# Kernel optimization log

Hardware: AMD Instinct MI355X
Metric: run time of the kernel (lower is better)

Reference implementation:

```python
import jax, jax.numpy as jnp
import numpy as np

# ---- dims (match init_kwargs / input_specs) ----
N = 20000      # nodes
E = 640000     # edges (avg degree 32)
A = 64         # num_node_feats (0e attrs)
F = 32         # num_features per irrep
B = 8          # num_bessel
H = 64         # radial MLP hidden
L = 2          # num_layers
NPATH = 5      # TP paths: s*Y0->0e, s*Y1->1e, v*Y0->1e, v.Y1->0e, v x Y1->1e
RMAX = 5.0
P = 6          # num_polynomial_cutoff
AVG = 32.0     # avg_num_neighbours


def setup_inputs() -> dict:
    key = jax.random.key(0)
    ks = jax.random.split(key, 11)
    node_attrs = jax.random.normal(ks[0], (N, A), jnp.float32)
    coordinates = jax.random.normal(ks[1], (N, 3), jnp.float32)
    edge_index = jax.random.randint(ks[2], (2, E), 0, N, dtype=jnp.int32)
    # learned params (e3nn-style fan-in init)
    node_emb_W = jax.random.normal(ks[3], (A, F), jnp.float32) * A ** -0.5
    rad_W1 = jax.random.normal(ks[4], (L, B, H), jnp.float32) * B ** -0.5
    rad_b1 = jnp.zeros((L, H), jnp.float32)
    rad_W2 = jax.random.normal(ks[5], (L, H, NPATH * F), jnp.float32) * H ** -0.5
    lin_Ws = jax.random.normal(ks[6], (L, F, 2 * F), jnp.float32) * F ** -0.5
    lin_Wv = jax.random.normal(ks[7], (L, F, F), jnp.float32) * F ** -0.5
    sc_Ws = jax.random.normal(ks[8], (L, F, A, 2 * F), jnp.float32) * (F * A) ** -0.5
    sc_Wv = jax.random.normal(ks[9], (L, F, A, F), jnp.float32) * (F * A) ** -0.5
    return {"node_attrs": node_attrs, "coordinates": coordinates, "edge_index": edge_index,
            "node_emb_W": node_emb_W, "rad_W1": rad_W1, "rad_b1": rad_b1, "rad_W2": rad_W2,
            "lin_Ws": lin_Ws, "lin_Wv": lin_Wv, "sc_Ws": sc_Ws, "sc_Wv": sc_Wv}


def _nequip_forward(node_attrs, coordinates, node_emb_W, rad_W1, rad_b1, rad_W2,
                    lin_Ws, lin_Wv, sc_Ws, sc_Wv, edge_index):
    snd, rcv = edge_index[0], edge_index[1]
    vec = coordinates[snd] - coordinates[rcv]                    # [E,3]
    r = jnp.sqrt(jnp.sum(vec * vec, -1) + 1e-12)                 # [E]
    unit = vec / r[:, None]
    x = r / RMAX
    # Bessel radial basis * polynomial cutoff (p=6)
    n = jnp.arange(1, B + 1, dtype=jnp.float32)
    bessel = jnp.sqrt(2.0 / RMAX) * jnp.sin(n[None, :] * jnp.pi * x[:, None]) / r[:, None]
    c1 = -(P + 1) * (P + 2) / 2.0
    c2 = float(P * (P + 2))
    c3 = -P * (P + 1) / 2.0
    fcut = (1.0 + c1 * x ** P + c2 * x ** (P + 1) + c3 * x ** (P + 2)) * (x < 1.0)
    edge_feats = bessel * fcut[:, None]                          # [E,B]
    # spherical harmonics, component normalization: Y0=1, Y1=sqrt(3)*r_hat
    Y1 = jnp.sqrt(3.0) * unit                                    # [E,3]
    # node embedding: 0e linear
    s = node_attrs @ node_emb_W                                  # [N,F] scalars (0e)
    v = jnp.zeros((N, F, 3), s.dtype)                            # [N,F,3] vectors (1e)
    inv = 1.0 / jnp.sqrt(AVG)
    for l in range(L):
        # radial MLP -> per-edge, per-path, per-channel TP weights
        h = jax.nn.silu(edge_feats @ rad_W1[l] + rad_b1[l])      # [E,H]
        w = (h @ rad_W2[l]).reshape(E, NPATH, F)                 # [E,5,F]
        s_j = s[snd]                                             # [E,F]
        v_j = v[snd]                                             # [E,F,3]
        Ye = Y1[:, None, :]                                      # [E,1,3]
        dot = jnp.sum(v_j * Ye, -1)                              # 1e x 1e -> 0e
        crs = jnp.cross(v_j, jnp.broadcast_to(Ye, v_j.shape))    # 1e x 1e -> 1e
        m_s = w[:, 0] * s_j + w[:, 3] * dot                      # [E,F]
        m_v = (w[:, 1, :, None] * s_j[:, :, None] * Ye
               + w[:, 2, :, None] * v_j
               + w[:, 4, :, None] * crs)                         # [E,F,3]
        agg_s = jax.ops.segment_sum(m_s, rcv, num_segments=N) * inv
        agg_v = jax.ops.segment_sum(m_v, rcv, num_segments=N) * inv
        # linear mixing + self-connection (feats x node_attrs tensor product)
        pre_s = (jnp.einsum('nf,fg->ng', agg_s, lin_Ws[l])
                 + jnp.einsum('nf,na,fag->ng', s, node_attrs, sc_Ws[l]))   # [N,2F]
        pre_v = (jnp.einsum('nfc,fg->ngc', agg_v, lin_Wv[l])
                 + jnp.einsum('nfc,na,fag->ngc', v, node_attrs, sc_Wv[l])) # [N,F,3]
        feats, gates = pre_s[:, :F], pre_s[:, F:]
        # gate nonlinearity + resnet
        s = jax.nn.silu(feats) + s
        v = pre_v * jax.nn.sigmoid(gates)[:, :, None] + v
    return jnp.concatenate([s, v.reshape(N, 3 * F)], axis=-1)   # [N,4F]


def reference(node_attrs, coordinates, edge_index, node_emb_W, rad_W1, rad_b1,
              rad_W2, lin_Ws, lin_Wv, sc_Ws, sc_Wv):
    return _nequip_forward(node_attrs, coordinates, node_emb_W, rad_W1, rad_b1,
                           rad_W2, lin_Ws, lin_Wv, sc_Ws, sc_Wv, edge_index)
```

## Files before the change

kernel.cpp:

```cpp
#include <hip/hip_runtime.h>
#include <hip/hip_bf16.h>

#define NN 20000
#define NE 640000

constexpr float INV_AVG = 0.17677669529663687f;
constexpr float SQRT3   = 1.7320508075688772f;
constexpr float BPREF   = 0.6324555320336759f;
constexpr float PI_F    = 3.14159265358979323846f;

__device__ __forceinline__ float sigmoidf_(float x) { return 1.0f / (1.0f + __expf(-x)); }

__global__ __launch_bounds__(256) void k_embed(const float* __restrict__ attrs,
                                               const float* __restrict__ W,
                                               float* __restrict__ s)
{
    int t = blockIdx.x * 256 + threadIdx.x;
    int n = t >> 5, f = t & 31;
    const float* ar = attrs + n * 64;
    float acc = 0.f;
    #pragma unroll
    for (int a = 0; a < 64; ++a) acc += ar[a] * W[a * 32 + f];
    s[t] = acc;
}

__global__ __launch_bounds__(256) void k_count(const int* __restrict__ ei, int* __restrict__ deg)
{
    int e = blockIdx.x * 256 + threadIdx.x;
    atomicAdd(&deg[ei[NE + e]], 1);
}

__global__ __launch_bounds__(256) void k_scan(const int* __restrict__ deg,
                                              int* __restrict__ base,
                                              int* __restrict__ cursor)
{
    __shared__ int part[256];
    int t = threadIdx.x;
    int start = t * 80;
    int s = 0;
    for (int i = 0; i < 80; ++i) { int n = start + i; if (n < NN) s += deg[n]; }
    part[t] = s;
    __syncthreads();
    for (int off = 1; off < 256; off <<= 1) {
        int v = (t >= off) ? part[t - off] : 0;
        __syncthreads();
        part[t] += v;
        __syncthreads();
    }
    int run = (t == 0) ? 0 : part[t - 1];
    for (int i = 0; i < 80; ++i) {
        int n = start + i;
        if (n < NN) { base[n] = run; cursor[n] = run; run += deg[n]; }
    }
    if (t == 255) base[NN] = run;
}

__global__ __launch_bounds__(256) void k_fill(const int* __restrict__ ei,
                                              int* __restrict__ cursor,
                                              int* __restrict__ eidx)
{
    int e = blockIdx.x * 256 + threadIdx.x;
    int slot = atomicAdd(&cursor[ei[NE + e]], 1);
    eidx[slot] = e;
}

__global__ __launch_bounds__(256) void k_edge_msg(const float* __restrict__ coords,
                                                  const int* __restrict__ ei,
                                                  const int* __restrict__ eidx,
                                                  const float* __restrict__ W1,
                                                  const float* __restrict__ b1,
                                                  const float* __restrict__ W2,
                                                  const float* __restrict__ s_cur,
                                                  const float* __restrict__ v_cur,
                                                  float* __restrict__ msg,
                                                  int c0, int c1)
{
    __shared__ float w2s[64 * 160];
    {
        const float4* src = reinterpret_cast<const float4*>(W2);
        float4* dst = reinterpret_cast<float4*>(w2s);
        #pragma unroll
        for (int i = 0; i < 10; ++i) dst[threadIdx.x + 256 * i] = src[threadIdx.x + 256 * i];
    }
    __syncthreads();

    int slot = c0 + blockIdx.x * 256 + threadIdx.x;
    if (slot >= c1) return;
    int e = eidx[slot];
    int snd = ei[e], rcv = ei[NE + e];

    float d0 = coords[snd * 3 + 0] - coords[rcv * 3 + 0];
    float d1 = coords[snd * 3 + 1] - coords[rcv * 3 + 1];
    float d2 = coords[snd * 3 + 2] - coords[rcv * 3 + 2];
    float r2 = d0 * d0 + d1 * d1 + d2 * d2 + 1e-12f;
    float r = sqrtf(r2);
    float rinv = 1.0f / r;
    float Y0 = SQRT3 * d0 * rinv, Y1 = SQRT3 * d1 * rinv, Y2 = SQRT3 * d2 * rinv;
    float x = r * 0.2f;

    float x2 = x * x, x3 = x2 * x, x6 = x3 * x3;
    float fc = 1.0f + x6 * (-28.0f + x * (48.0f - 21.0f * x));
    fc = (x < 1.0f) ? fc : 0.0f;
    float scale = BPREF * rinv * fc;

    float s1, c1s;
    __sincosf(PI_F * x, &s1, &c1s);
    float ef[8];
    float sp = 0.f, sc = s1, twoc = 2.f * c1s;
    ef[0] = sc * scale;
    #pragma unroll
    for (int n = 1; n < 8; ++n) { float nx = twoc * sc - sp; sp = sc; sc = nx; ef[n] = sc * scale; }

    float h[64];
    #pragma unroll
    for (int j = 0; j < 64; ++j) {
        float acc = b1[j];
        #pragma unroll
        for (int b = 0; b < 8; ++b) acc += ef[b] * W1[b * 64 + j];
        h[j] = acc * sigmoidf_(acc);
    }

    const float* srow = s_cur + snd * 32;
    const float* vrow = v_cur + snd * 96;
    float* mout = msg + (size_t)(slot - c0) * 128;

    for (int f0 = 0; f0 < 32; f0 += 4) {
        float acc[5][4];
        #pragma unroll
        for (int p = 0; p < 5; ++p) { acc[p][0] = 0.f; acc[p][1] = 0.f; acc[p][2] = 0.f; acc[p][3] = 0.f; }
        #pragma unroll
        for (int j = 0; j < 64; ++j) {
            float hj = h[j];
            #pragma unroll
            for (int p = 0; p < 5; ++p) {
                const float4 wv = *reinterpret_cast<const float4*>(&w2s[j * 160 + p * 32 + f0]);
                acc[p][0] += hj * wv.x; acc[p][1] += hj * wv.y;
                acc[p][2] += hj * wv.z; acc[p][3] += hj * wv.w;
            }
        }
        float ms[4], mv[12];
        #pragma unroll
        for (int i = 0; i < 4; ++i) {
            int f = f0 + i;
            float sj = srow[f];
            float v0 = vrow[f * 3 + 0], v1 = vrow[f * 3 + 1], v2 = vrow[f * 3 + 2];
            float dot = v0 * Y0 + v1 * Y1 + v2 * Y2;
            float cr0 = v1 * Y2 - v2 * Y1;
            float cr1 = v2 * Y0 - v0 * Y2;
            float cr2 = v0 * Y1 - v1 * Y0;
            ms[i]        = acc[0][i] * sj + acc[3][i] * dot;
            float t1     = acc[1][i] * sj;
            mv[i * 3 + 0] = t1 * Y0 + acc[2][i] * v0 + acc[4][i] * cr0;
            mv[i * 3 + 1] = t1 * Y1 + acc[2][i] * v1 + acc[4][i] * cr1;
            mv[i * 3 + 2] = t1 * Y2 + acc[2][i] * v2 + acc[4][i] * cr2;
        }
        *reinterpret_cast<float4*>(mout + f0) = make_float4(ms[0], ms[1], ms[2], ms[3]);
        float4* vv = reinterpret_cast<float4*>(mout + 32 + f0 * 3);
        vv[0] = make_float4(mv[0], mv[1], mv[2], mv[3]);
        vv[1] = make_float4(mv[4], mv[5], mv[6], mv[7]);
        vv[2] = make_float4(mv[8], mv[9], mv[10], mv[11]);
    }
}

__global__ __launch_bounds__(256) void k_gather(const float* __restrict__ msg,
                                                const int* __restrict__ base,
                                                float* __restrict__ agg_s,
                                                float* __restrict__ agg_v,
                                                int c0, int c1)
{
    int t = threadIdx.x & 127;
    int n = (blockIdx.x << 1) | (threadIdx.x >> 7);
    if (n >= NN) return;
    int b0 = base[n], b1 = base[n + 1];
    int lo = b0 > c0 ? b0 : c0;
    int hi = b1 < c1 ? b1 : c1;
    if (lo >= hi) return;
    float acc = 0.f;
    for (int i = lo; i < hi; ++i) acc += msg[(size_t)(i - c0) * 128 + t];
    acc *= INV_AVG;
    if (t < 32) agg_s[n * 32 + t] += acc;
    else        agg_v[n * 96 + (t - 32)] += acc;
}

__global__ __launch_bounds__(512) void k_node_s(const float* __restrict__ attrs,
                                                const float* __restrict__ s_cur,
                                                const float* __restrict__ agg_s,
                                                const float* __restrict__ scWs,
                                                const float* __restrict__ linWs,
                                                float* __restrict__ s_next,
                                                float* __restrict__ gate)
{
    int wave = threadIdx.x >> 6;
    int l    = threadIdx.x & 63;
    int g0   = __builtin_amdgcn_readfirstlane(wave * 4);
    int n    = blockIdx.x * 64 + l;
    int nc   = (n < NN) ? n : (NN - 1);

    float ar[64];
    #pragma unroll
    for (int i = 0; i < 16; ++i) {
        const float4 v = *reinterpret_cast<const float4*>(&attrs[nc * 64 + i * 4]);
        ar[i * 4 + 0] = v.x; ar[i * 4 + 1] = v.y; ar[i * 4 + 2] = v.z; ar[i * 4 + 3] = v.w;
    }

    float lo0 = 0.f, lo1 = 0.f, lo2 = 0.f, lo3 = 0.f;
    float hi0 = 0.f, hi1 = 0.f, hi2 = 0.f, hi3 = 0.f;
    const float* sr = s_cur + (size_t)nc * 32;
    for (int f = 0; f < 32; ++f) {
        float sf = sr[f];
        const float* wrow = scWs + ((size_t)f * 64) * 64;
        #pragma unroll
        for (int a = 0; a < 64; ++a) {
            float o = sf * ar[a];
            const float4 wl = *reinterpret_cast<const float4*>(wrow + a * 64 + g0);
            const float4 wh = *reinterpret_cast<const float4*>(wrow + a * 64 + g0 + 32);
            lo0 += o * wl.x; lo1 += o * wl.y; lo2 += o * wl.z; lo3 += o * wl.w;
            hi0 += o * wh.x; hi1 += o * wh.y; hi2 += o * wh.z; hi3 += o * wh.w;
        }
    }
    const float* gr = agg_s + (size_t)nc * 32;
    #pragma unroll
    for (int f = 0; f < 32; ++f) {
        float av = gr[f];
        const float4 wl = *reinterpret_cast<const float4*>(linWs + f * 64 + g0);
        const float4 wh = *reinterpret_cast<const float4*>(linWs + f * 64 + g0 + 32);
        lo0 += av * wl.x; lo1 += av * wl.y; lo2 += av * wl.z; lo3 += av * wl.w;
        hi0 += av * wh.x; hi1 += av * wh.y; hi2 += av * wh.z; hi3 += av * wh.w;
    }

    if (n < NN) {
        float los[4] = {lo0, lo1, lo2, lo3};
        float his[4] = {hi0, hi1, hi2, hi3};
        #pragma unroll
        for (int j = 0; j < 4; ++j) {
            int g = g0 + j;
            float pre = los[j];
            s_next[n * 32 + g] = pre * sigmoidf_(pre) + s_cur[n * 32 + g];
            gate[n * 32 + g]   = sigmoidf_(his[j]);
        }
    }
}

__global__ __launch_bounds__(512) void k_node_v(const float* __restrict__ attrs,
                                                const float* __restrict__ v_cur,
                                                const float* __restrict__ agg_v,
                                                const float* __restrict__ scWv,
                                                const float* __restrict__ linWv,
                                                const float* __restrict__ gate,
                                                float* __restrict__ v_next)
{
    int wave = threadIdx.x >> 6;
    int l    = threadIdx.x & 63;
    int g0   = __builtin_amdgcn_readfirstlane(wave * 4);
    int n    = blockIdx.x * 64 + l;
    int nc   = (n < NN) ? n : (NN - 1);

    float ar[64];
    #pragma unroll
    for (int i = 0; i < 16; ++i) {
        const float4 v = *reinterpret_cast<const float4*>(&attrs[nc * 64 + i * 4]);
        ar[i * 4 + 0] = v.x; ar[i * 4 + 1] = v.y; ar[i * 4 + 2] = v.z; ar[i * 4 + 3] = v.w;
    }

    float acc[4][3] = {};
    const float* vr = v_cur + (size_t)nc * 96;
    for (int f = 0; f < 32; ++f) {
        float v0 = vr[f * 3 + 0], v1 = vr[f * 3 + 1], v2 = vr[f * 3 + 2];
        const float* wrow = scWv + ((size_t)f * 64) * 32 + g0;
        #pragma unroll
        for (int a = 0; a < 64; ++a) {
            const float4 wv = *reinterpret_cast<const float4*>(wrow + a * 32);
            float at = ar[a];
            float o0 = at * v0, o1 = at * v1, o2 = at * v2;
            acc[0][0] += o0 * wv.x; acc[0][1] += o1 * wv.x; acc[0][2] += o2 * wv.x;
            acc[1][0] += o0 * wv.y; acc[1][1] += o1 * wv.y; acc[1][2] += o2 * wv.y;
            acc[2][0] += o0 * wv.z; acc[2][1] += o1 * wv.z; acc[2][2] += o2 * wv.z;
            acc[3][0] += o0 * wv.w; acc[3][1] += o1 * wv.w; acc[3][2] += o2 * wv.w;
        }
    }
    const float* gr = agg_v + (size_t)nc * 96;
    #pragma unroll
    for (int f = 0; f < 32; ++f) {
        float q0 = gr[f * 3 + 0], q1 = gr[f * 3 + 1], q2 = gr[f * 3 + 2];
        const float4 wv = *reinterpret_cast<const float4*>(linWv + f * 32 + g0);
        acc[0][0] += q0 * wv.x; acc[0][1] += q1 * wv.x; acc[0][2] += q2 * wv.x;
        acc[1][0] += q0 * wv.y; acc[1][1] += q1 * wv.y; acc[1][2] += q2 * wv.y;
        acc[2][0] += q0 * wv.z; acc[2][1] += q1 * wv.z; acc[2][2] += q2 * wv.z;
        acc[3][0] += q0 * wv.w; acc[3][1] += q1 * wv.w; acc[3][2] += q2 * wv.w;
    }

    if (n < NN) {
        #pragma unroll
        for (int j = 0; j < 4; ++j) {
            int g = g0 + j;
            float gt = gate[n * 32 + g];
            #pragma unroll
            for (int c = 0; c < 3; ++c) {
                int idx = (n * 32 + g) * 3 + c;
                v_next[idx] = acc[j][c] * gt + v_cur[idx];
            }
        }
    }
}

__global__ __launch_bounds__(256) void k_out(const float* __restrict__ s,
                                             const float* __restrict__ v,
                                             float* __restrict__ out)
{
    int t = blockIdx.x * 256 + threadIdx.x;
    int n = t >> 7, i = t & 127;
    float val = (i < 32) ? s[n * 32 + i] : v[n * 96 + (i - 32)];
    out[t] = val;
}

extern "C" void kernel_launch(void* const* d_in, const int* in_sizes, int n_in,
                              void* d_out, int out_size, void* d_ws, size_t ws_size,
                              hipStream_t stream)
{
    const float* attrs  = (const float*)d_in[0];
    const float* coords = (const float*)d_in[1];
    const int*   ei     = (const int*)d_in[2];
    const float* embW   = (const float*)d_in[3];
    const float* radW1  = (const float*)d_in[4];
    const float* radb1  = (const float*)d_in[5];
    const float* radW2  = (const float*)d_in[6];
    const float* linWs  = (const float*)d_in[7];
    const float* linWv  = (const float*)d_in[8];
    const float* scWs   = (const float*)d_in[9];
    const float* scWv   = (const float*)d_in[10];
    float* out = (float*)d_out;

    float* ws = (float*)d_ws;
    const size_t NS = (size_t)NN * 32, NV = (size_t)NN * 96;
    float* s_a   = ws;
    float* s_b   = s_a + NS;
    float* v_a   = s_b + NS;
    float* v_b   = v_a + NV;
    float* agg_s = v_b + NV;
    float* agg_v = agg_s + NS;
    float* gate  = agg_v + NV;
    int*   ip    = (int*)(gate + NS);
    int*   deg    = ip;
    int*   basep  = deg + NN;
    int*   cursor = basep + NN + 1;
    int*   eidx   = cursor + NN;
    float* msg   = (float*)(ip + 700004);

    const size_t fixedBytes = (size_t)((char*)msg - (char*)ws);
    size_t avail = (ws_size > fixedBytes) ? (ws_size - fixedBytes) : 0;
    long long cap = (long long)(avail / (128 * sizeof(float)));
    int C = (int)(cap > NE ? NE : cap);
    C &= ~255;
    const bool use_csr = (C >= 256);

    hipMemsetAsync(v_a, 0, NV * sizeof(float), stream);
    k_embed<<<2500, 256, 0, stream>>>(attrs, embW, s_a);

    if (use_csr) {
        hipMemsetAsync(deg, 0, NN * sizeof(int), stream);
        k_count<<<NE / 256, 256, 0, stream>>>(ei, deg);
        k_scan<<<1, 256, 0, stream>>>(deg, basep, cursor);
        k_fill<<<NE / 256, 256, 0, stream>>>(ei, cursor, eidx);
    }

    float* scur = s_a; float* snext = s_b;
    float* vcur = v_a; float* vnext = v_b;
    for (int l = 0; l < 2; ++l) {
        hipMemsetAsync(agg_s, 0, (NS + NV) * sizeof(float), stream);
        if (use_csr) {
            for (int c0 = 0; c0 < NE; c0 += C) {
                int c1 = (c0 + C < NE) ? (c0 + C) : NE;
                int len = c1 - c0;
                k_edge_msg<<<(len + 255) / 256, 256, 0, stream>>>(coords, ei, eidx,
                    radW1 + l * 8 * 64, radb1 + l * 64, radW2 + l * 64 * 160,
                    scur, vcur, msg, c0, c1);
                k_gather<<<NN / 2, 256, 0, stream>>>(msg, basep, agg_s, agg_v, c0, c1);
            }
        }
        k_node_s<<<313, 512, 0, stream>>>(attrs, scur, agg_s,
            scWs + l * 32 * 64 * 64, linWs + l * 32 * 64, snext, gate);
        k_node_v<<<313, 512, 0, stream>>>(attrs, vcur, agg_v,
            scWv + l * 32 * 64 * 32, linWv + l * 32 * 32, gate, vnext);
        float* tt = scur; scur = snext; snext = tt;
        tt = vcur; vcur = vnext; vnext = tt;
    }
    k_out<<<10000, 256, 0, stream>>>(scur, vcur, out);
}
```

Measured before the change: 2.539 ms.

## Fuse edge message computation with in-block segmented reduction into aggregates

Replaces the write-messages-then-gather scheme with a single edge kernel that reduces messages per receiver inside each block through shared memory. Receivers fully contained in a block are stored directly, and boundary receivers use atomic adds. This removes the 128-float-per-edge message buffer round trip through global memory and the separate gather launch. The cost is extra shared memory, which lowers occupancy, plus extra syncthreads per feature chunk and serial run scans. A fallback kernel using per-edge atomics is added for when the workspace is too small.

```diff
diff --git a/kernel.cpp b/kernel.cpp
--- a/kernel.cpp
+++ b/kernel.cpp
@@ -64,30 +64,44 @@
     eidx[slot] = e;
 }
 
-__global__ __launch_bounds__(256) void k_edge_msg(const float* __restrict__ coords,
+__global__ __launch_bounds__(256) void k_edge_red(const float* __restrict__ coords,
                                                   const int* __restrict__ ei,
                                                   const int* __restrict__ eidx,
+                                                  const int* __restrict__ basep,
                                                   const float* __restrict__ W1,
                                                   const float* __restrict__ b1,
                                                   const float* __restrict__ W2,
                                                   const float* __restrict__ s_cur,
                                                   const float* __restrict__ v_cur,
-                                                  float* __restrict__ msg,
-                                                  int c0, int c1)
+                                                  float* __restrict__ agg_s,
+                                                  float* __restrict__ agg_v)
 {
     __shared__ float w2s[64 * 160];
+    __shared__ float red[16 * 257];
+    __shared__ int   rcvs[256];
+    __shared__ int   runStart[257];
+    __shared__ int   runCnt;
+
+    int t = threadIdx.x;
     {
         const float4* src = reinterpret_cast<const float4*>(W2);
         float4* dst = reinterpret_cast<float4*>(w2s);
         #pragma unroll
-        for (int i = 0; i < 10; ++i) dst[threadIdx.x + 256 * i] = src[threadIdx.x + 256 * i];
-    }
-    __syncthreads();
-
-    int slot = c0 + blockIdx.x * 256 + threadIdx.x;
-    if (slot >= c1) return;
+        for (int i = 0; i < 10; ++i) dst[t + 256 * i] = src[t + 256 * i];
+    }
+    if (t == 0) runCnt = 0;
+
+    int s0 = blockIdx.x * 256;
+    int slot = s0 + t;
     int e = eidx[slot];
     int snd = ei[e], rcv = ei[NE + e];
+    rcvs[t] = rcv;
+    __syncthreads();
+
+    if (t == 0 || rcvs[t] != rcvs[t - 1]) {
+        int idx = atomicAdd(&runCnt, 1);
+        runStart[idx] = t;
+    }
 
     float d0 = coords[snd * 3 + 0] - coords[rcv * 3 + 0];
     float d1 = coords[snd * 3 + 1] - coords[rcv * 3 + 1];
@@ -122,7 +136,6 @@
 
     const float* srow = s_cur + snd * 32;
     const float* vrow = v_cur + snd * 96;
-    float* mout = msg + (size_t)(slot - c0) * 128;
 
     for (int f0 = 0; f0 < 32; f0 += 4) {
         float acc[5][4];
@@ -138,7 +151,7 @@
                 acc[p][2] += hj * wv.z; acc[p][3] += hj * wv.w;
             }
         }
-        float ms[4], mv[12];
+        __syncthreads();
         #pragma unroll
         for (int i = 0; i < 4; ++i) {
             int f = f0 + i;
@@ -148,38 +161,126 @@
             float cr0 = v1 * Y2 - v2 * Y1;
             float cr1 = v2 * Y0 - v0 * Y2;
             float cr2 = v0 * Y1 - v1 * Y0;
-            ms[i]        = acc[0][i] * sj + acc[3][i] * dot;
-            float t1     = acc[1][i] * sj;
-            mv[i * 3 + 0] = t1 * Y0 + acc[2][i] * v0 + acc[4][i] * cr0;
-            mv[i * 3 + 1] = t1 * Y1 + acc[2][i] * v1 + acc[4][i] * cr1;
-            mv[i * 3 + 2] = t1 * Y2 + acc[2][i] * v2 + acc[4][i] * cr2;
-        }
-        *reinterpret_cast<float4*>(mout + f0) = make_float4(ms[0], ms[1], ms[2], ms[3]);
-        float4* vv = reinterpret_cast<float4*>(mout + 32 + f0 * 3);
-        vv[0] = make_float4(mv[0], mv[1], mv[2], mv[3]);
-        vv[1] = make_float4(mv[4], mv[5], mv[6], mv[7]);
-        vv[2] = make_float4(mv[8], mv[9], mv[10], mv[11]);
-    }
-}
-
-__global__ __launch_bounds__(256) void k_gather(const float* __restrict__ msg,
-                                                const int* __restrict__ base,
-                                                float* __restrict__ agg_s,
-                                                float* __restrict__ agg_v,
-                                                int c0, int c1)
-{
-    int t = threadIdx.x & 127;
-    int n = (blockIdx.x << 1) | (threadIdx.x >> 7);
-    if (n >= NN) return;
-    int b0 = base[n], b1 = base[n + 1];
-    int lo = b0 > c0 ? b0 : c0;
-    int hi = b1 < c1 ? b1 : c1;
-    if (lo >= hi) return;
-    float acc = 0.f;
-    for (int i = lo; i < hi; ++i) acc += msg[(size_t)(i - c0) * 128 + t];
-    acc *= INV_AVG;
-    if (t < 32) agg_s[n * 32 + t] += acc;
-    else        agg_v[n * 96 + (t - 32)] += acc;
+            red[i * 257 + t]            = acc[0][i] * sj + acc[3][i] * dot;
+            float t1                    = acc[1][i] * sj;
+            red[(4 + i * 3 + 0) * 257 + t] = t1 * Y0 + acc[2][i] * v0 + acc[4][i] * cr0;
+            red[(4 + i * 3 + 1) * 257 + t] = t1 * Y1 + acc[2][i] * v1 + acc[4][i] * cr1;
+            red[(4 + i * 3 + 2) * 257 + t] = t1 * Y2 + acc[2][i] * v2 + acc[4][i] * cr2;
+        }
+        __syncthreads();
+        int nr = runCnt;
+        int c = t & 15;
+        for (int rr = t >> 4; rr < nr; rr += 16) {
+            int rs = runStart[rr];
+            int n = rcvs[rs];
+            int re = rs + 1;
+            while (re < 256 && rcvs[re] == n) ++re;
+            float sum = 0.f;
+            for (int i2 = rs; i2 < re; ++i2) sum += red[c * 257 + i2];
+            sum *= INV_AVG;
+            int gb0 = basep[n], gb1 = basep[n + 1];
+            bool complete = (gb0 >= s0) && (gb1 <= s0 + 256);
+            float* dst;
+            if (c < 4) dst = &agg_s[n * 32 + f0 + c];
+            else { int j = c - 4; dst = &agg_v[n * 96 + (f0 + j / 3) * 3 + (j % 3)]; }
+            if (complete) *dst = sum;
+            else unsafeAtomicAdd(dst, sum);
+        }
+    }
+}
+
+__global__ __launch_bounds__(256) void k_edge(const float* __restrict__ coords,
+                                              const int* __restrict__ ei,
+                                              const float* __restrict__ W1,
+                                              const float* __restrict__ b1,
+                                              const float* __restrict__ W2,
+                                              const float* __restrict__ s_cur,
+                                              const float* __restrict__ v_cur,
+                                              float* __restrict__ agg_s,
+                                              float* __restrict__ agg_v)
+{
+    __shared__ float w2s[64 * 160];
+    {
+        const float4* src = reinterpret_cast<const float4*>(W2);
+        float4* dst = reinterpret_cast<float4*>(w2s);
+        #pragma unroll
+        for (int i = 0; i < 10; ++i) dst[threadIdx.x + 256 * i] = src[threadIdx.x + 256 * i];
+    }
+    __syncthreads();
+
+    int e = blockIdx.x * 256 + threadIdx.x;
+    int snd = ei[e], rcv = ei[NE + e];
+
+    float d0 = coords[snd * 3 + 0] - coords[rcv * 3 + 0];
+    float d1 = coords[snd * 3 + 1] - coords[rcv * 3 + 1];
+    float d2 = coords[snd * 3 + 2] - coords[rcv * 3 + 2];
+    float r2 = d0 * d0 + d1 * d1 + d2 * d2 + 1e-12f;
+    float r = sqrtf(r2);
+    float rinv = 1.0f / r;
+    float Y0 = SQRT3 * d0 * rinv, Y1 = SQRT3 * d1 * rinv, Y2 = SQRT3 * d2 * rinv;
+    float x = r * 0.2f;
+
+    float x2 = x * x, x3 = x2 * x, x6 = x3 * x3;
+    float fc = 1.0f + x6 * (-28.0f + x * (48.0f - 21.0f * x));
+    fc = (x < 1.0f) ? fc : 0.0f;
+    float scale = BPREF * rinv * fc;
+
+    float s1, c1;
+    __sincosf(PI_F * x, &s1, &c1);
+    float ef[8];
+    float sp = 0.f, sc = s1, twoc = 2.f * c1;
+    ef[0] = sc * scale;
+    #pragma unroll
+    for (int n = 1; n < 8; ++n) { float nx = twoc * sc - sp; sp = sc; sc = nx; ef[n] = sc * scale; }
+
+    float h[64];
+    #pragma unroll
+    for (int j = 0; j < 64; ++j) {
+        float acc = b1[j];
+        #pragma unroll
+        for (int b = 0; b < 8; ++b) acc += ef[b] * W1[b * 64 + j];
+        h[j] = acc * sigmoidf_(acc);
+    }
+
+    const float* srow = s_cur + snd * 32;
+    const float* vrow = v_cur + snd * 96;
+    float* as = agg_s + rcv * 32;
+    float* av = agg_v + rcv * 96;
+
+    for (int f0 = 0; f0 < 32; f0 += 4) {
+        float acc[5][4];
+        #pragma unroll
+        for (int p = 0; p < 5; ++p) { acc[p][0] = 0.f; acc[p][1] = 0.f; acc[p][2] = 0.f; acc[p][3] = 0.f; }
+        #pragma unroll
+        for (int j = 0; j < 64; ++j) {
+            float hj = h[j];
+            #pragma unroll
+            for (int p = 0; p < 5; ++p) {
+                const float4 wv = *reinterpret_cast<const float4*>(&w2s[j * 160 + p * 32 + f0]);
+                acc[p][0] += hj * wv.x; acc[p][1] += hj * wv.y;
+                acc[p][2] += hj * wv.z; acc[p][3] += hj * wv.w;
+            }
+        }
+        #pragma unroll
+        for (int i = 0; i < 4; ++i) {
+            int f = f0 + i;
+            float sj = srow[f];
+            float v0 = vrow[f * 3 + 0], v1 = vrow[f * 3 + 1], v2 = vrow[f * 3 + 2];
+            float dot = v0 * Y0 + v1 * Y1 + v2 * Y2;
+            float cr0 = v1 * Y2 - v2 * Y1;
+            float cr1 = v2 * Y0 - v0 * Y2;
+            float cr2 = v0 * Y1 - v1 * Y0;
+            float ms  = (acc[0][i] * sj + acc[3][i] * dot) * INV_AVG;
+            float t1  = acc[1][i] * sj;
+            float mv0 = (t1 * Y0 + acc[2][i] * v0 + acc[4][i] * cr0) * INV_AVG;
+            float mv1 = (t1 * Y1 + acc[2][i] * v1 + acc[4][i] * cr1) * INV_AVG;
+            float mv2 = (t1 * Y2 + acc[2][i] * v2 + acc[4][i] * cr2) * INV_AVG;
+            unsafeAtomicAdd(as + f, ms);
+            unsafeAtomicAdd(av + f * 3 + 0, mv0);
+            unsafeAtomicAdd(av + f * 3 + 1, mv1);
+            unsafeAtomicAdd(av + f * 3 + 2, mv2);
+        }
+    }
 }
 
 __global__ __launch_bounds__(512) void k_node_s(const float* __restrict__ attrs,
@@ -344,14 +445,9 @@
     int*   basep  = deg + NN;
     int*   cursor = basep + NN + 1;
     int*   eidx   = cursor + NN;
-    float* msg   = (float*)(ip + 700004);
-
-    const size_t fixedBytes = (size_t)((char*)msg - (char*)ws);
-    size_t avail = (ws_size > fixedBytes) ? (ws_size - fixedBytes) : 0;
-    long long cap = (long long)(avail / (128 * sizeof(float)));
-    int C = (int)(cap > NE ? NE : cap);
-    C &= ~255;
-    const bool use_csr = (C >= 256);
+
+    const size_t required = (size_t)((char*)(eidx + NE) - (char*)ws);
+    const bool use_csr = ws_size >= required;
 
     hipMemsetAsync(v_a, 0, NV * sizeof(float), stream);
     k_embed<<<2500, 256, 0, stream>>>(attrs, embW, s_a);
@@ -368,14 +464,13 @@
     for (int l = 0; l < 2; ++l) {
         hipMemsetAsync(agg_s, 0, (NS + NV) * sizeof(float), stream);
         if (use_csr) {
-            for (int c0 = 0; c0 < NE; c0 += C) {
-                int c1 = (c0 + C < NE) ? (c0 + C) : NE;
-                int len = c1 - c0;
-                k_edge_msg<<<(len + 255) / 256, 256, 0, stream>>>(coords, ei, eidx,
-                    radW1 + l * 8 * 64, radb1 + l * 64, radW2 + l * 64 * 160,
-                    scur, vcur, msg, c0, c1);
-                k_gather<<<NN / 2, 256, 0, stream>>>(msg, basep, agg_s, agg_v, c0, c1);
-            }
+            k_edge_red<<<NE / 256, 256, 0, stream>>>(coords, ei, eidx, basep,
+                radW1 + l * 8 * 64, radb1 + l * 64, radW2 + l * 64 * 160,
+                scur, vcur, agg_s, agg_v);
+        } else {
+            k_edge<<<NE / 256, 256, 0, stream>>>(coords, ei,
+                radW1 + l * 8 * 64, radb1 + l * 64, radW2 + l * 64 * 160,
+                scur, vcur, agg_s, agg_v);
         }
         k_node_s<<<313, 512, 0, stream>>>(attrs, scur, agg_s,
             scWs + l * 32 * 64 * 64, linWs + l * 32 * 64, snext, gate);
```

New measurement: 2.219 ms. -12.6%, faster.
